# Performance work log

Hardware: AMD Instinct MI355X
Metric: run time of the kernel (lower is better)

Reference implementation:

```python
import jax, jax.numpy as jnp
import numpy as np

D_MODEL = 256
D_STATE = 16
D_CONV = 3
D_INNER = 256          # expand=1
D_HALF = D_INNER // 2  # 128
DT_RANK = 16           # ceil(256/16)
B, L0, L1 = 4, 4096, 4096


def setup_inputs() -> dict:
    key = jax.random.key(0)
    ks = jax.random.split(key, 10)
    u_0 = jax.random.normal(ks[0], (B, L0, D_MODEL), jnp.float32)
    u_1 = jax.random.normal(ks[1], (B, L1, D_MODEL), jnp.float32)
    in_proj_w = jax.random.normal(ks[2], (D_INNER, D_MODEL), jnp.float32) * (D_MODEL ** -0.5)
    conv_x_w = jax.random.normal(ks[3], (D_HALF, 1, D_CONV), jnp.float32) * (D_CONV ** -0.5)
    conv_z_w = jax.random.normal(ks[4], (D_HALF, 1, D_CONV), jnp.float32) * (D_CONV ** -0.5)
    x_proj_w = jax.random.normal(ks[5], (DT_RANK + 2 * D_STATE, D_HALF), jnp.float32) * (D_HALF ** -0.5)
    dt_init_std = DT_RANK ** -0.5
    dt_proj_w = jax.random.uniform(ks[6], (D_HALF, DT_RANK), jnp.float32, -dt_init_std, dt_init_std)
    # dt bias = inverse-softplus of dt ~ LogUniform(1e-3, 1e-1)
    dt = jnp.exp(jax.random.uniform(ks[7], (D_HALF,), jnp.float32) * (np.log(0.1) - np.log(0.001)) + np.log(0.001))
    dt = jnp.clip(dt, 1e-4, None)
    dt_proj_b = dt + jnp.log(-jnp.expm1(-dt))
    A_log = jnp.log(jnp.broadcast_to(jnp.arange(1, D_STATE + 1, dtype=jnp.float32), (D_HALF, D_STATE)))
    D_param = jnp.ones((D_HALF,), jnp.float32)
    out_proj_w = jax.random.normal(ks[8], (D_MODEL, D_INNER), jnp.float32) * (D_INNER ** -0.5)
    return {"u_0": u_0, "u_1": u_1, "in_proj_w": in_proj_w, "conv_x_w": conv_x_w,
            "conv_z_w": conv_z_w, "x_proj_w": x_proj_w, "dt_proj_w": dt_proj_w,
            "dt_proj_b": dt_proj_b, "A_log": A_log, "D": D_param, "out_proj_w": out_proj_w}


def _dwconv(x, w):
    # x: [B, C, L], w: [C, 1, K] depthwise, padding='same', no bias (conv_bias//2 == 0)
    return jax.lax.conv_general_dilated(
        x, w, window_strides=(1,), padding='SAME',
        feature_group_count=x.shape[1], dimension_numbers=('NCH', 'OIH', 'NCH'))


def _selective_scan(u, delta, A, Bm, Cm, Dv):
    # u, delta: [B, L, d]; A: [d, n]; Bm, Cm: [B, L, n]; Dv: [d]
    dA = jnp.exp(delta[..., None] * A)                       # [B, L, d, n]
    dBu = (delta * u)[..., None] * Bm[:, :, None, :]         # [B, L, d, n]
    def combine(c1, c2):
        a1, b1 = c1
        a2, b2 = c2
        return a2 * a1, a2 * b1 + b2
    _, h = jax.lax.associative_scan(combine, (dA, dBu), axis=1)  # h: [B, L, d, n]
    return jnp.einsum('bldn,bln->bld', h, Cm) + u * Dv


def _stream(u, in_proj_w, conv_x_w, conv_z_w, x_proj_w, dt_proj_w, dt_proj_b, A, D, out_proj_w):
    xz = jnp.einsum('bld,ed->ble', u, in_proj_w)             # [B, L, d_inner]
    x, z = jnp.split(xz, 2, axis=-1)                         # [B, L, d_half] each
    x = jnp.swapaxes(x, 1, 2)                                # [B, d_half, L]
    z = jnp.swapaxes(z, 1, 2)
    x_f = jax.nn.silu(_dwconv(x, conv_x_w))
    z_f = jax.nn.silu(_dwconv(z, conv_z_w))
    xf = jnp.swapaxes(x_f, 1, 2)                             # [B, L, d_half]
    dbl = jnp.einsum('bld,ed->ble', xf, x_proj_w)            # [B, L, dt_rank + 2n]
    dt, Bm, Cm = jnp.split(dbl, [DT_RANK, DT_RANK + D_STATE], axis=-1)
    dt = jnp.einsum('blr,dr->bld', dt, dt_proj_w)
    delta = jax.nn.softplus(dt + dt_proj_b)                  # delta_bias + delta_softplus
    y = _selective_scan(xf, delta, A, Bm, Cm, D)             # [B, L, d_half]
    cat = jnp.concatenate([y, jnp.swapaxes(z_f, 1, 2)], axis=-1)  # [B, L, d_inner]
    return jnp.einsum('ble,oe->blo', cat, out_proj_w)


def reference(u_0, u_1, in_proj_w, conv_x_w, conv_z_w, x_proj_w, dt_proj_w, dt_proj_b, A_log, D, out_proj_w):
    A = -jnp.exp(A_log)
    out0 = _stream(u_0, in_proj_w, conv_x_w, conv_z_w, x_proj_w, dt_proj_w, dt_proj_b, A, D, out_proj_w)
    out1 = _stream(u_1, in_proj_w, conv_x_w, conv_z_w, x_proj_w, dt_proj_w, dt_proj_b, A, D, out_proj_w)
    return (out0, out1)
```

## Files before the change

### kernel.cpp

```cpp
#include <hip/hip_runtime.h>
#include <hip/hip_bf16.h>
#include <cstdint>

#define DEV __device__ __forceinline__

typedef __attribute__((ext_vector_type(8))) short short8;
typedef __attribute__((ext_vector_type(4))) float f32x4;
typedef __attribute__((ext_vector_type(4))) unsigned short us4;
typedef __attribute__((ext_vector_type(8))) unsigned short us8;

DEV unsigned short f2bf(float x) {
    unsigned int u = __float_as_uint(x);
    unsigned int r = (u + 0x7FFFu + ((u >> 16) & 1u)) >> 16;
    return (unsigned short)r;
}
DEV float bf2f(unsigned short h) { return __uint_as_float(((unsigned int)h) << 16); }

DEV void gld_lds16(const unsigned short* g, unsigned short* l) {
    __builtin_amdgcn_global_load_lds(
        (const __attribute__((address_space(1))) unsigned int*)g,
        (__attribute__((address_space(3))) unsigned int*)l, 16, 0, 0);
}

#define LL 4096
#define DM 256
#define DH 128
#define NS 16
#define SB_TOT 8
#define CH1 32
#define NCH 128
#define LOG2E 1.44269504088896f

__global__ __launch_bounds__(256) void prep_kernel(
    const float* __restrict__ u0, const float* __restrict__ u1,
    const float* __restrict__ inw, const float* __restrict__ outw,
    const float* __restrict__ xpw, const float* __restrict__ dtw,
    unsigned short* __restrict__ ubf, unsigned short* __restrict__ wbi,
    unsigned short* __restrict__ wbo, unsigned short* __restrict__ Wb)
{
    int gid = blockIdx.x * 256 + threadIdx.x;
    int i = gid * 4;
    if (i < 4194304) {
        f32x4 v = *(const f32x4*)&u0[i];
        us4 r = { f2bf(v.x), f2bf(v.y), f2bf(v.z), f2bf(v.w) };
        *(us4*)&ubf[i] = r;
    } else if (i < 8388608) {
        int j = i - 4194304;
        f32x4 v = *(const f32x4*)&u1[j];
        us4 r = { f2bf(v.x), f2bf(v.y), f2bf(v.z), f2bf(v.w) };
        *(us4*)&ubf[4194304 + j] = r;
    } else if (i < 8454144) {
        int j = i - 8388608;
        f32x4 v = *(const f32x4*)&inw[j];
        us4 r = { f2bf(v.x), f2bf(v.y), f2bf(v.z), f2bf(v.w) };
        *(us4*)&wbi[j] = r;
    } else if (i < 8519680) {
        int j = i - 8454144;
        f32x4 v = *(const f32x4*)&outw[j];
        us4 r = { f2bf(v.x), f2bf(v.y), f2bf(v.z), f2bf(v.w) };
        *(us4*)&wbo[j] = r;
    } else if (i < 8540160) {
        int j = i - 8519680;
        int n = j >> 7, k0 = j & 127;
        if (n < 128) {
            float a0 = 0.f, a1 = 0.f, a2 = 0.f, a3 = 0.f;
            const float* dw = dtw + n * 16;
            #pragma unroll
            for (int r = 0; r < 16; ++r) {
                float w = dw[r];
                const float* xr = xpw + r * 128 + k0;
                a0 = fmaf(w, xr[0], a0);
                a1 = fmaf(w, xr[1], a1);
                a2 = fmaf(w, xr[2], a2);
                a3 = fmaf(w, xr[3], a3);
            }
            us4 rr = { f2bf(a0), f2bf(a1), f2bf(a2), f2bf(a3) };
            *(us4*)&Wb[n * 128 + k0] = rr;
        } else {
            f32x4 v = *(const f32x4*)&xpw[(n - 112) * 128 + k0];
            us4 rr = { f2bf(v.x), f2bf(v.y), f2bf(v.z), f2bf(v.w) };
            *(us4*)&Wb[n * 128 + k0] = rr;
        }
    }
}

template<int F32OUT>
__global__ __launch_bounds__(256) void gemm_bt(
    const unsigned short* __restrict__ A, const unsigned short* __restrict__ B,
    float* __restrict__ Cf, unsigned short* __restrict__ Cb)
{
    __shared__ __align__(16) unsigned short As[128 * 32];
    __shared__ __align__(16) unsigned short Bs[128 * 32];
    const int t = threadIdx.x;
    const int m0 = blockIdx.x * 128, n0 = blockIdx.y * 128;
    const int lane = t & 63, wv = t >> 6;
    const int wm = (wv & 1) * 64, wn = (wv >> 1) * 64;
    const int lr = lane & 15, lk = (lane >> 4) * 8;
    const int srow = lane >> 2, scol = (lane & 3) * 8;

    f32x4 acc[4][4] = {};
    for (int kt = 0; kt < 8; ++kt) {
        const int k0 = kt * 32;
        #pragma unroll
        for (int h = 0; h < 2; ++h) {
            const int c = wv + h * 4;
            const unsigned short* ga = A + (size_t)(m0 + c * 16 + srow) * 256 + k0 + scol;
            const unsigned short* gb = B + (size_t)(n0 + c * 16 + srow) * 256 + k0 + scol;
            gld_lds16(ga, &As[c * 512]);
            gld_lds16(gb, &Bs[c * 512]);
        }
        __syncthreads();
        short8 av[4], bv[4];
        #pragma unroll
        for (int i = 0; i < 4; ++i) av[i] = *(const short8*)&As[(wm + i * 16 + lr) * 32 + lk];
        #pragma unroll
        for (int i = 0; i < 4; ++i) bv[i] = *(const short8*)&Bs[(wn + i * 16 + lr) * 32 + lk];
        #pragma unroll
        for (int i = 0; i < 4; ++i)
            #pragma unroll
            for (int j = 0; j < 4; ++j)
                acc[i][j] = __builtin_amdgcn_mfma_f32_16x16x32_bf16(av[i], bv[j], acc[i][j], 0, 0, 0);
        __syncthreads();
    }
    #pragma unroll
    for (int i = 0; i < 4; ++i) {
        #pragma unroll
        for (int j = 0; j < 4; ++j) {
            int r0 = m0 + wm + i * 16 + (lane >> 4) * 4;
            int cc = n0 + wn + j * 16 + lr;
            #pragma unroll
            for (int r = 0; r < 4; ++r) {
                float v = acc[i][j][r];
                if (F32OUT) Cf[(size_t)(r0 + r) * 256 + cc] = v;
                else        Cb[(size_t)(r0 + r) * 256 + cc] = f2bf(v);
            }
        }
    }
}

__global__ __launch_bounds__(256) void convproj(
    const unsigned short* __restrict__ xz, const unsigned short* __restrict__ Wb,
    const float* __restrict__ wx, const float* __restrict__ wz,
    const float* __restrict__ dtb,
    float* __restrict__ xf, unsigned short* __restrict__ catb,
    float* __restrict__ delta, float* __restrict__ BC)
{
    __shared__ __align__(16) unsigned short Bs[160 * 136];
    __shared__ __align__(16) unsigned short As[64 * 136];
    const int t = threadIdx.x;
    const int m0 = blockIdx.x * 64;
    for (int q = t; q < 2560; q += 256) {
        int n = q >> 4, kc = (q & 15) * 8;
        *(short8*)&Bs[n * 136 + kc] = *(const short8*)(Wb + n * 128 + kc);
    }
    #pragma unroll
    for (int i = 0; i < 8; ++i) {
        int s = t + i * 256;
        int r = s >> 5, g = s & 31;
        int gr = m0 + r;
        int l = gr & 4095;
        int c; const float* wp; const unsigned short* bp;
        if (g < 16) { c = g * 8;        wp = wx; bp = xz + (size_t)gr * 256 + c; }
        else        { c = (g - 16) * 8; wp = wz; bp = xz + (size_t)gr * 256 + 128 + c; }
        us8 zz = (us8)0;
        us8 vm = (l > 0)    ? *(const us8*)(bp - 256) : zz;
        us8 v0 = *(const us8*)bp;
        us8 vp = (l < 4095) ? *(const us8*)(bp + 256) : zz;
        float o[8];
        #pragma unroll
        for (int j = 0; j < 8; ++j) {
            int cc = c + j;
            float v = bf2f(vm[j]) * wp[cc * 3] + bf2f(v0[j]) * wp[cc * 3 + 1]
                    + bf2f(vp[j]) * wp[cc * 3 + 2];
            v = v / (1.f + __expf(-v));
            o[j] = v;
        }
        us8 rb = { f2bf(o[0]), f2bf(o[1]), f2bf(o[2]), f2bf(o[3]),
                   f2bf(o[4]), f2bf(o[5]), f2bf(o[6]), f2bf(o[7]) };
        if (g < 16) {
            *(us8*)&As[r * 136 + c] = rb;
            *(f32x4*)&xf[(size_t)gr * 128 + c]     = *(f32x4*)&o[0];
            *(f32x4*)&xf[(size_t)gr * 128 + c + 4] = *(f32x4*)&o[4];
        } else {
            *(us8*)&catb[(size_t)gr * 256 + 128 + c] = rb;
        }
    }
    __syncthreads();
    const int lane = t & 63, wv = t >> 6;
    const int lr = lane & 15, lk = (lane >> 4) * 8;
    f32x4 acc[10] = {};
    #pragma unroll
    for (int kt = 0; kt < 4; ++kt) {
        const int k0 = kt * 32;
        short8 av = *(const short8*)&As[(wv * 16 + lr) * 136 + k0 + lk];
        #pragma unroll
        for (int j = 0; j < 10; ++j) {
            short8 bv = *(const short8*)&Bs[(j * 16 + lr) * 136 + k0 + lk];
            acc[j] = __builtin_amdgcn_mfma_f32_16x16x32_bf16(av, bv, acc[j], 0, 0, 0);
        }
    }
    const int r0 = (lane >> 4) * 4;
    #pragma unroll
    for (int j = 0; j < 10; ++j) {
        int col = j * 16 + lr;
        #pragma unroll
        for (int r = 0; r < 4; ++r) {
            float v = acc[j][r];
            size_t row = (size_t)m0 + wv * 16 + r0 + r;
            if (j < 8) {
                float x = v + dtb[col];
                float sp = (x > 20.f) ? x : log1pf(__expf(x));
                delta[row * 128 + col] = sp;
            } else {
                BC[row * 32 + (col - 128)] = v;
            }
        }
    }
}

__global__ __launch_bounds__(128) void scan_p1(
    const float* __restrict__ delta, const float* __restrict__ xf,
    const float* __restrict__ BC, const float* __restrict__ alog,
    float* __restrict__ P, float* __restrict__ H)
{
    __shared__ float dt_s[CH1 * 128];
    __shared__ float du_s[CH1 * 128];
    __shared__ float b_s[CH1 * 16];
    int t = threadIdx.x;
    int ch = blockIdx.x, sb = blockIdx.y;
    size_t rb = (size_t)sb * LL + (size_t)ch * CH1;
    for (int q = t; q < CH1 * 32; q += 128) {
        int row = q >> 5, c4 = (q & 31) * 4;
        f32x4 dv = *(const f32x4*)&delta[(rb + row) * DH + c4];
        f32x4 uv = *(const f32x4*)&xf[(rb + row) * DH + c4];
        *(f32x4*)&dt_s[row * 128 + c4] = dv;
        f32x4 duv = dv * uv;
        *(f32x4*)&du_s[row * 128 + c4] = duv;
    }
    {
        int q = t & 127;
        int row = q >> 2, c4 = (q & 3) * 4;
        *(f32x4*)&b_s[row * 16 + c4] = *(const f32x4*)&BC[(rb + row) * 32 + c4];
    }
    __syncthreads();
    float Ar[16];
    #pragma unroll
    for (int n = 0; n < 16; ++n) Ar[n] = -__expf(alog[t * 16 + n]) * LOG2E;
    float h[16], p[16];
    #pragma unroll
    for (int n = 0; n < 16; ++n) { h[n] = 0.f; p[n] = 1.f; }
    for (int i = 0; i < CH1; ++i) {
        float dt = dt_s[i * 128 + t];
        float du = du_s[i * 128 + t];
        float bl[16];
        *(f32x4*)&bl[0]  = *(const f32x4*)&b_s[i * 16];
        *(f32x4*)&bl[4]  = *(const f32x4*)&b_s[i * 16 + 4];
        *(f32x4*)&bl[8]  = *(const f32x4*)&b_s[i * 16 + 8];
        *(f32x4*)&bl[12] = *(const f32x4*)&b_s[i * 16 + 12];
        #pragma unroll
        for (int n = 0; n < 16; ++n) {
            float a = exp2f(dt * Ar[n]);
            h[n] = fmaf(a, h[n], du * bl[n]);
            p[n] *= a;
        }
    }
    size_t ob = (((size_t)sb * NCH + ch) * 128 + t) * 16;
    #pragma unroll
    for (int n4 = 0; n4 < 16; n4 += 4) {
        f32x4 pv = { p[n4], p[n4 + 1], p[n4 + 2], p[n4 + 3] };
        f32x4 hv = { h[n4], h[n4 + 1], h[n4 + 2], h[n4 + 3] };
        *(f32x4*)&P[ob + n4] = pv;
        *(f32x4*)&H[ob + n4] = hv;
    }
}

__global__ __launch_bounds__(256) void scan_p2(const float* __restrict__ P, float* __restrict__ H)
{
    __shared__ float Ps[NCH * 16], Hs[NCH * 16];
    int t = threadIdx.x;
    int d = blockIdx.x, sb = blockIdx.y;
    for (int q = t; q < NCH * 4; q += 256) {
        int ch = q >> 2, c4 = (q & 3) * 4;
        size_t g = (((size_t)sb * NCH + ch) * 128 + d) * 16 + c4;
        *(f32x4*)&Ps[ch * 16 + c4] = *(const f32x4*)&P[g];
        *(f32x4*)&Hs[ch * 16 + c4] = *(const f32x4*)&H[g];
    }
    __syncthreads();
    if (t < 16) {
        float hin = 0.f;
        for (int c = 0; c < NCH; ++c) {
            float pp = Ps[c * 16 + t], hl = Hs[c * 16 + t];
            Hs[c * 16 + t] = hin;
            hin = fmaf(pp, hin, hl);
        }
    }
    __syncthreads();
    for (int q = t; q < NCH * 4; q += 256) {
        int ch = q >> 2, c4 = (q & 3) * 4;
        size_t g = (((size_t)sb * NCH + ch) * 128 + d) * 16 + c4;
        *(f32x4*)&H[g] = *(const f32x4*)&Hs[ch * 16 + c4];
    }
}

__global__ __launch_bounds__(128) void scan_p3(
    const float* __restrict__ delta, const float* __restrict__ xf,
    const float* __restrict__ BC, const float* __restrict__ alog,
    const float* __restrict__ Dp, const float* __restrict__ H,
    unsigned short* __restrict__ catb)
{
    __shared__ float dt_s[CH1 * 128];
    __shared__ float u_s[CH1 * 128];
    __shared__ float b_s[CH1 * 16];
    __shared__ float c_s[CH1 * 16];
    int t = threadIdx.x;
    int ch = blockIdx.x, sb = blockIdx.y;
    size_t rb = (size_t)sb * LL + (size_t)ch * CH1;
    for (int q = t; q < CH1 * 32; q += 128) {
        int row = q >> 5, c4 = (q & 31) * 4;
        *(f32x4*)&dt_s[row * 128 + c4] = *(const f32x4*)&delta[(rb + row) * DH + c4];
        *(f32x4*)&u_s[row * 128 + c4]  = *(const f32x4*)&xf[(rb + row) * DH + c4];
    }
    {
        int q = t & 127;
        int row = q >> 2, c4 = (q & 3) * 4;
        *(f32x4*)&b_s[row * 16 + c4] = *(const f32x4*)&BC[(rb + row) * 32 + c4];
        *(f32x4*)&c_s[row * 16 + c4] = *(const f32x4*)&BC[(rb + row) * 32 + 16 + c4];
    }
    __syncthreads();
    float Ar[16];
    #pragma unroll
    for (int n = 0; n < 16; ++n) Ar[n] = -__expf(alog[t * 16 + n]) * LOG2E;
    float Dv = Dp[t];
    size_t ob = (((size_t)sb * NCH + ch) * 128 + t) * 16;
    float h[16];
    #pragma unroll
    for (int n4 = 0; n4 < 16; n4 += 4) {
        f32x4 hv = *(const f32x4*)&H[ob + n4];
        h[n4] = hv.x; h[n4 + 1] = hv.y; h[n4 + 2] = hv.z; h[n4 + 3] = hv.w;
    }
    for (int i = 0; i < CH1; ++i) {
        float dt = dt_s[i * 128 + t];
        float uu = u_s[i * 128 + t];
        float du = dt * uu;
        float bl[16], cl[16];
        *(f32x4*)&bl[0]  = *(const f32x4*)&b_s[i * 16];
        *(f32x4*)&bl[4]  = *(const f32x4*)&b_s[i * 16 + 4];
        *(f32x4*)&bl[8]  = *(const f32x4*)&b_s[i * 16 + 8];
        *(f32x4*)&bl[12] = *(const f32x4*)&b_s[i * 16 + 12];
        *(f32x4*)&cl[0]  = *(const f32x4*)&c_s[i * 16];
        *(f32x4*)&cl[4]  = *(const f32x4*)&c_s[i * 16 + 4];
        *(f32x4*)&cl[8]  = *(const f32x4*)&c_s[i * 16 + 8];
        *(f32x4*)&cl[12] = *(const f32x4*)&c_s[i * 16 + 12];
        float y0 = uu * Dv, y1 = 0.f, y2 = 0.f, y3 = 0.f;
        #pragma unroll
        for (int n = 0; n < 16; n += 4) {
            float a0 = exp2f(dt * Ar[n]);
            float a1 = exp2f(dt * Ar[n + 1]);
            float a2 = exp2f(dt * Ar[n + 2]);
            float a3 = exp2f(dt * Ar[n + 3]);
            h[n]     = fmaf(a0, h[n],     du * bl[n]);
            h[n + 1] = fmaf(a1, h[n + 1], du * bl[n + 1]);
            h[n + 2] = fmaf(a2, h[n + 2], du * bl[n + 2]);
            h[n + 3] = fmaf(a3, h[n + 3], du * bl[n + 3]);
            y0 = fmaf(h[n],     cl[n],     y0);
            y1 = fmaf(h[n + 1], cl[n + 1], y1);
            y2 = fmaf(h[n + 2], cl[n + 2], y2);
            y3 = fmaf(h[n + 3], cl[n + 3], y3);
        }
        float y = (y0 + y1) + (y2 + y3);
        catb[(rb + i) * DM + t] = f2bf(y);
    }
}

extern "C" void kernel_launch(void* const* d_in, const int* in_sizes, int n_in,
                              void* d_out, int out_size, void* d_ws, size_t ws_size,
                              hipStream_t stream) {
    const float* u0   = (const float*)d_in[0];
    const float* u1   = (const float*)d_in[1];
    const float* inw  = (const float*)d_in[2];
    const float* cxw  = (const float*)d_in[3];
    const float* czw  = (const float*)d_in[4];
    const float* xpw  = (const float*)d_in[5];
    const float* dtw  = (const float*)d_in[6];
    const float* dtb  = (const float*)d_in[7];
    const float* alog = (const float*)d_in[8];
    const float* Dp   = (const float*)d_in[9];
    const float* outw = (const float*)d_in[10];

    char* ws = (char*)d_ws;
    unsigned short* ubf  = (unsigned short*)(ws + 0);
    float* delta         = (float*)(ws + 0);
    unsigned short* xzbf = (unsigned short*)(ws + 16777216);
    float* P             = (float*)(ws + 16777216);
    float* H             = (float*)(ws + 25165824);
    float* xf            = (float*)(ws + 33554432);
    float* BC            = (float*)(ws + 50331648);
    unsigned short* catb = (unsigned short*)(ws + 54525952);
    unsigned short* wbi  = (unsigned short*)(ws + 71303168);
    unsigned short* wbo  = (unsigned short*)(ws + 71434240);
    unsigned short* Wb   = (unsigned short*)(ws + 71565312);

    float* outp = (float*)d_out;

    prep_kernel<<<8340, 256, 0, stream>>>(u0, u1, inw, outw, xpw, dtw, ubf, wbi, wbo, Wb);
    gemm_bt<0><<<dim3(256, 2), 256, 0, stream>>>(ubf, wbi, nullptr, xzbf);
    convproj<<<512, 256, 0, stream>>>(xzbf, Wb, cxw, czw, dtb, xf, catb, delta, BC);
    scan_p1<<<dim3(NCH, 8), 128, 0, stream>>>(delta, xf, BC, alog, P, H);
    scan_p2<<<dim3(128, 8), 256, 0, stream>>>(P, H);
    scan_p3<<<dim3(NCH, 8), 128, 0, stream>>>(delta, xf, BC, alog, Dp, H, catb);
    gemm_bt<1><<<dim3(256, 2), 256, 0, stream>>>(catb, wbo, outp, nullptr);
}
```

Baseline: 224.7 us.

## Fuse all stages into one persistent kernel with grid-wide atomic barriers

Replaces the seven separate launches (prep, two GEMMs, conv/projection, three scan phases) with a single persistent 512-block kernel whose stages are separated by software grid barriers built on atomic counters. It also keeps delta and x in registers between scan phase 1 and phase 3, so they are not reloaded, and reads the projection weights from global memory instead of staging them in LDS. The aim is to remove launch gaps and repeated loads. In exchange the barriers spin and serialize the stages, the barrier is only safe if all 512 blocks are resident at once, and shared-memory reuse through a union may limit occupancy.

```diff
diff --git a/kernel.cpp b/kernel.cpp
--- a/kernel.cpp
+++ b/kernel.cpp
@@ -25,74 +25,44 @@
 #define LL 4096
 #define DM 256
 #define DH 128
-#define NS 16
 #define SB_TOT 8
 #define CH1 32
 #define NCH 128
 #define LOG2E 1.44269504088896f
-
-__global__ __launch_bounds__(256) void prep_kernel(
-    const float* __restrict__ u0, const float* __restrict__ u1,
-    const float* __restrict__ inw, const float* __restrict__ outw,
-    const float* __restrict__ xpw, const float* __restrict__ dtw,
-    unsigned short* __restrict__ ubf, unsigned short* __restrict__ wbi,
-    unsigned short* __restrict__ wbo, unsigned short* __restrict__ Wb)
+#define NBLK 512
+
+DEV void gbar(unsigned int* cnt, int idx) {
+    __syncthreads();
+    if (threadIdx.x == 0) {
+        __threadfence();
+        __hip_atomic_fetch_add(&cnt[idx], 1u, __ATOMIC_ACQ_REL, __HIP_MEMORY_SCOPE_AGENT);
+        while (__hip_atomic_load(&cnt[idx], __ATOMIC_ACQUIRE, __HIP_MEMORY_SCOPE_AGENT) < (unsigned)NBLK) {
+            __builtin_amdgcn_s_sleep(4);
+        }
+        __threadfence();
+    }
+    __syncthreads();
+}
+
+__global__ __launch_bounds__(64) void bar_init(unsigned int* cnt) {
+    if (threadIdx.x < 16) cnt[threadIdx.x] = 0u;
+}
+
+union SMU {
+    struct { unsigned short As[128 * 32]; unsigned short Bs[128 * 32]; } g;
+    struct { unsigned short As[64 * 136]; } c;
+    struct { float b_s[2][512]; float c_s[2][512];
+             float Ps[2][2048]; float Hs[2][2048]; } s;
+};
+
+template<int F32OUT>
+DEV void gemm_phase(SMU* sm, int blk, int t,
+                    const unsigned short* A, const unsigned short* B,
+                    float* Cf, unsigned short* Cb)
 {
-    int gid = blockIdx.x * 256 + threadIdx.x;
-    int i = gid * 4;
-    if (i < 4194304) {
-        f32x4 v = *(const f32x4*)&u0[i];
-        us4 r = { f2bf(v.x), f2bf(v.y), f2bf(v.z), f2bf(v.w) };
-        *(us4*)&ubf[i] = r;
-    } else if (i < 8388608) {
-        int j = i - 4194304;
-        f32x4 v = *(const f32x4*)&u1[j];
-        us4 r = { f2bf(v.x), f2bf(v.y), f2bf(v.z), f2bf(v.w) };
-        *(us4*)&ubf[4194304 + j] = r;
-    } else if (i < 8454144) {
-        int j = i - 8388608;
-        f32x4 v = *(const f32x4*)&inw[j];
-        us4 r = { f2bf(v.x), f2bf(v.y), f2bf(v.z), f2bf(v.w) };
-        *(us4*)&wbi[j] = r;
-    } else if (i < 8519680) {
-        int j = i - 8454144;
-        f32x4 v = *(const f32x4*)&outw[j];
-        us4 r = { f2bf(v.x), f2bf(v.y), f2bf(v.z), f2bf(v.w) };
-        *(us4*)&wbo[j] = r;
-    } else if (i < 8540160) {
-        int j = i - 8519680;
-        int n = j >> 7, k0 = j & 127;
-        if (n < 128) {
-            float a0 = 0.f, a1 = 0.f, a2 = 0.f, a3 = 0.f;
-            const float* dw = dtw + n * 16;
-            #pragma unroll
-            for (int r = 0; r < 16; ++r) {
-                float w = dw[r];
-                const float* xr = xpw + r * 128 + k0;
-                a0 = fmaf(w, xr[0], a0);
-                a1 = fmaf(w, xr[1], a1);
-                a2 = fmaf(w, xr[2], a2);
-                a3 = fmaf(w, xr[3], a3);
-            }
-            us4 rr = { f2bf(a0), f2bf(a1), f2bf(a2), f2bf(a3) };
-            *(us4*)&Wb[n * 128 + k0] = rr;
-        } else {
-            f32x4 v = *(const f32x4*)&xpw[(n - 112) * 128 + k0];
-            us4 rr = { f2bf(v.x), f2bf(v.y), f2bf(v.z), f2bf(v.w) };
-            *(us4*)&Wb[n * 128 + k0] = rr;
-        }
-    }
-}
-
-template<int F32OUT>
-__global__ __launch_bounds__(256) void gemm_bt(
-    const unsigned short* __restrict__ A, const unsigned short* __restrict__ B,
-    float* __restrict__ Cf, unsigned short* __restrict__ Cb)
-{
-    __shared__ __align__(16) unsigned short As[128 * 32];
-    __shared__ __align__(16) unsigned short Bs[128 * 32];
-    const int t = threadIdx.x;
-    const int m0 = blockIdx.x * 128, n0 = blockIdx.y * 128;
+    unsigned short* As = sm->g.As;
+    unsigned short* Bs = sm->g.Bs;
+    const int m0 = (blk >> 1) * 128, n0 = (blk & 1) * 128;
     const int lane = t & 63, wv = t >> 6;
     const int wm = (wv & 1) * 64, wn = (wv >> 1) * 64;
     const int lr = lane & 15, lk = (lane >> 4) * 8;
@@ -138,238 +108,260 @@
     }
 }
 
-__global__ __launch_bounds__(256) void convproj(
-    const unsigned short* __restrict__ xz, const unsigned short* __restrict__ Wb,
-    const float* __restrict__ wx, const float* __restrict__ wz,
-    const float* __restrict__ dtb,
-    float* __restrict__ xf, unsigned short* __restrict__ catb,
-    float* __restrict__ delta, float* __restrict__ BC)
+__global__ __launch_bounds__(256, 2) void mamba_all(
+    const float* u0, const float* u1, const float* inw,
+    const float* cxw, const float* czw, const float* xpw,
+    const float* dtw, const float* dtb, const float* alog,
+    const float* Dp, const float* outw,
+    unsigned short* ubf, unsigned short* wbi, unsigned short* wbo,
+    unsigned short* Wb, unsigned short* xzbf, float* xf,
+    unsigned short* catb, float* delta, float* BC,
+    float* P, float* H, float* outp, unsigned int* cnt)
 {
-    __shared__ __align__(16) unsigned short Bs[160 * 136];
-    __shared__ __align__(16) unsigned short As[64 * 136];
     const int t = threadIdx.x;
-    const int m0 = blockIdx.x * 64;
-    for (int q = t; q < 2560; q += 256) {
-        int n = q >> 4, kc = (q & 15) * 8;
-        *(short8*)&Bs[n * 136 + kc] = *(const short8*)(Wb + n * 128 + kc);
+    const int b = blockIdx.x;
+    __shared__ __align__(16) SMU sm;
+
+    for (int it = 0; it < 17; ++it) {
+        int i = (b * 256 + t + it * 131072) * 4;
+        if (i >= 8540160) break;
+        if (i < 4194304) {
+            f32x4 v = *(const f32x4*)&u0[i];
+            us4 r = { f2bf(v.x), f2bf(v.y), f2bf(v.z), f2bf(v.w) };
+            *(us4*)&ubf[i] = r;
+        } else if (i < 8388608) {
+            int j = i - 4194304;
+            f32x4 v = *(const f32x4*)&u1[j];
+            us4 r = { f2bf(v.x), f2bf(v.y), f2bf(v.z), f2bf(v.w) };
+            *(us4*)&ubf[4194304 + j] = r;
+        } else if (i < 8454144) {
+            int j = i - 8388608;
+            f32x4 v = *(const f32x4*)&inw[j];
+            us4 r = { f2bf(v.x), f2bf(v.y), f2bf(v.z), f2bf(v.w) };
+            *(us4*)&wbi[j] = r;
+        } else if (i < 8519680) {
+            int j = i - 8454144;
+            f32x4 v = *(const f32x4*)&outw[j];
+            us4 r = { f2bf(v.x), f2bf(v.y), f2bf(v.z), f2bf(v.w) };
+            *(us4*)&wbo[j] = r;
+        } else {
+            int j = i - 8519680;
+            int n = j >> 7, k0 = j & 127;
+            if (n < 128) {
+                float a0 = 0.f, a1 = 0.f, a2 = 0.f, a3 = 0.f;
+                const float* dw = dtw + n * 16;
+                #pragma unroll
+                for (int r = 0; r < 16; ++r) {
+                    float w = dw[r];
+                    const float* xr = xpw + r * 128 + k0;
+                    a0 = fmaf(w, xr[0], a0);
+                    a1 = fmaf(w, xr[1], a1);
+                    a2 = fmaf(w, xr[2], a2);
+                    a3 = fmaf(w, xr[3], a3);
+                }
+                us4 rr = { f2bf(a0), f2bf(a1), f2bf(a2), f2bf(a3) };
+                *(us4*)&Wb[n * 128 + k0] = rr;
+            } else {
+                f32x4 v = *(const f32x4*)&xpw[(n - 112) * 128 + k0];
+                us4 rr = { f2bf(v.x), f2bf(v.y), f2bf(v.z), f2bf(v.w) };
+                *(us4*)&Wb[n * 128 + k0] = rr;
+            }
+        }
+    }
+    gbar(cnt, 0);
+
+    gemm_phase<0>(&sm, b, t, ubf, wbi, nullptr, xzbf);
+    gbar(cnt, 1);
+
+    {
+        const int m0 = b * 64;
+        #pragma unroll
+        for (int i = 0; i < 8; ++i) {
+            int s = t + i * 256;
+            int r = s >> 5, g = s & 31;
+            int gr = m0 + r;
+            int l = gr & 4095;
+            int c; const float* wp; const unsigned short* bp;
+            if (g < 16) { c = g * 8;        wp = cxw; bp = xzbf + (size_t)gr * 256 + c; }
+            else        { c = (g - 16) * 8; wp = czw; bp = xzbf + (size_t)gr * 256 + 128 + c; }
+            us8 zz = (us8)0;
+            us8 vm = (l > 0)    ? *(const us8*)(bp - 256) : zz;
+            us8 v0 = *(const us8*)bp;
+            us8 vp = (l < 4095) ? *(const us8*)(bp + 256) : zz;
+            float o[8];
+            #pragma unroll
+            for (int j = 0; j < 8; ++j) {
+                int cc = c + j;
+                float v = bf2f(vm[j]) * wp[cc * 3] + bf2f(v0[j]) * wp[cc * 3 + 1]
+                        + bf2f(vp[j]) * wp[cc * 3 + 2];
+                v = v / (1.f + __expf(-v));
+                o[j] = v;
+            }
+            us8 rb8 = { f2bf(o[0]), f2bf(o[1]), f2bf(o[2]), f2bf(o[3]),
+                        f2bf(o[4]), f2bf(o[5]), f2bf(o[6]), f2bf(o[7]) };
+            if (g < 16) {
+                *(us8*)&sm.c.As[r * 136 + c] = rb8;
+                *(f32x4*)&xf[(size_t)gr * 128 + c]     = *(f32x4*)&o[0];
+                *(f32x4*)&xf[(size_t)gr * 128 + c + 4] = *(f32x4*)&o[4];
+            } else {
+                *(us8*)&catb[(size_t)gr * 256 + 128 + c] = rb8;
+            }
+        }
+        __syncthreads();
+        const int lane = t & 63, wv = t >> 6;
+        const int lr = lane & 15, lk = (lane >> 4) * 8;
+        f32x4 acc[10] = {};
+        #pragma unroll
+        for (int kt = 0; kt < 4; ++kt) {
+            const int k0 = kt * 32;
+            short8 av = *(const short8*)&sm.c.As[(wv * 16 + lr) * 136 + k0 + lk];
+            #pragma unroll
+            for (int j = 0; j < 10; ++j) {
+                short8 bv = *(const short8*)(Wb + (j * 16 + lr) * 128 + k0 + lk);
+                acc[j] = __builtin_amdgcn_mfma_f32_16x16x32_bf16(av, bv, acc[j], 0, 0, 0);
+            }
+        }
+        const int r0 = (lane >> 4) * 4;
+        #pragma unroll
+        for (int j = 0; j < 10; ++j) {
+            int col = j * 16 + lr;
+            #pragma unroll
+            for (int r = 0; r < 4; ++r) {
+                float v = acc[j][r];
+                size_t row = (size_t)m0 + wv * 16 + r0 + r;
+                if (j < 8) {
+                    float x = v + dtb[col];
+                    float sp = (x > 20.f) ? x : log1pf(__expf(x));
+                    delta[row * 128 + col] = sp;
+                } else {
+                    BC[row * 32 + (col - 128)] = v;
+                }
+            }
+        }
+    }
+    gbar(cnt, 2);
+
+    const int hh = t >> 7, tl = t & 127;
+    const int task = 2 * b + hh;
+    const int sb = task >> 7, ch = task & 127;
+    const size_t rb = (size_t)sb * LL + (size_t)ch * CH1;
+    float dtr[32], ur[32];
+    {
+        int row = tl >> 2, c4 = (tl & 3) * 4;
+        *(f32x4*)&sm.s.b_s[hh][row * 16 + c4] = *(const f32x4*)&BC[(rb + row) * 32 + c4];
+        *(f32x4*)&sm.s.c_s[hh][row * 16 + c4] = *(const f32x4*)&BC[(rb + row) * 32 + 16 + c4];
     }
     #pragma unroll
-    for (int i = 0; i < 8; ++i) {
-        int s = t + i * 256;
-        int r = s >> 5, g = s & 31;
-        int gr = m0 + r;
-        int l = gr & 4095;
-        int c; const float* wp; const unsigned short* bp;
-        if (g < 16) { c = g * 8;        wp = wx; bp = xz + (size_t)gr * 256 + c; }
-        else        { c = (g - 16) * 8; wp = wz; bp = xz + (size_t)gr * 256 + 128 + c; }
-        us8 zz = (us8)0;
-        us8 vm = (l > 0)    ? *(const us8*)(bp - 256) : zz;
-        us8 v0 = *(const us8*)bp;
-        us8 vp = (l < 4095) ? *(const us8*)(bp + 256) : zz;
-        float o[8];
-        #pragma unroll
-        for (int j = 0; j < 8; ++j) {
-            int cc = c + j;
-            float v = bf2f(vm[j]) * wp[cc * 3] + bf2f(v0[j]) * wp[cc * 3 + 1]
-                    + bf2f(vp[j]) * wp[cc * 3 + 2];
-            v = v / (1.f + __expf(-v));
-            o[j] = v;
-        }
-        us8 rb = { f2bf(o[0]), f2bf(o[1]), f2bf(o[2]), f2bf(o[3]),
-                   f2bf(o[4]), f2bf(o[5]), f2bf(o[6]), f2bf(o[7]) };
-        if (g < 16) {
-            *(us8*)&As[r * 136 + c] = rb;
-            *(f32x4*)&xf[(size_t)gr * 128 + c]     = *(f32x4*)&o[0];
-            *(f32x4*)&xf[(size_t)gr * 128 + c + 4] = *(f32x4*)&o[4];
-        } else {
-            *(us8*)&catb[(size_t)gr * 256 + 128 + c] = rb;
-        }
-    }
+    for (int i = 0; i < 32; ++i) dtr[i] = delta[(rb + i) * DH + tl];
+    #pragma unroll
+    for (int i = 0; i < 32; ++i) ur[i] = xf[(rb + i) * DH + tl];
     __syncthreads();
-    const int lane = t & 63, wv = t >> 6;
-    const int lr = lane & 15, lk = (lane >> 4) * 8;
-    f32x4 acc[10] = {};
-    #pragma unroll
-    for (int kt = 0; kt < 4; ++kt) {
-        const int k0 = kt * 32;
-        short8 av = *(const short8*)&As[(wv * 16 + lr) * 136 + k0 + lk];
-        #pragma unroll
-        for (int j = 0; j < 10; ++j) {
-            short8 bv = *(const short8*)&Bs[(j * 16 + lr) * 136 + k0 + lk];
-            acc[j] = __builtin_amdgcn_mfma_f32_16x16x32_bf16(av, bv, acc[j], 0, 0, 0);
-        }
-    }
-    const int r0 = (lane >> 4) * 4;
-    #pragma unroll
-    for (int j = 0; j < 10; ++j) {
-        int col = j * 16 + lr;
-        #pragma unroll
-        for (int r = 0; r < 4; ++r) {
-            float v = acc[j][r];
-            size_t row = (size_t)m0 + wv * 16 + r0 + r;
-            if (j < 8) {
-                float x = v + dtb[col];
-                float sp = (x > 20.f) ? x : log1pf(__expf(x));
-                delta[row * 128 + col] = sp;
-            } else {
-                BC[row * 32 + (col - 128)] = v;
-            }
-        }
-    }
-}
-
-__global__ __launch_bounds__(128) void scan_p1(
-    const float* __restrict__ delta, const float* __restrict__ xf,
-    const float* __restrict__ BC, const float* __restrict__ alog,
-    float* __restrict__ P, float* __restrict__ H)
-{
-    __shared__ float dt_s[CH1 * 128];
-    __shared__ float du_s[CH1 * 128];
-    __shared__ float b_s[CH1 * 16];
-    int t = threadIdx.x;
-    int ch = blockIdx.x, sb = blockIdx.y;
-    size_t rb = (size_t)sb * LL + (size_t)ch * CH1;
-    for (int q = t; q < CH1 * 32; q += 128) {
-        int row = q >> 5, c4 = (q & 31) * 4;
-        f32x4 dv = *(const f32x4*)&delta[(rb + row) * DH + c4];
-        f32x4 uv = *(const f32x4*)&xf[(rb + row) * DH + c4];
-        *(f32x4*)&dt_s[row * 128 + c4] = dv;
-        f32x4 duv = dv * uv;
-        *(f32x4*)&du_s[row * 128 + c4] = duv;
-    }
     {
-        int q = t & 127;
-        int row = q >> 2, c4 = (q & 3) * 4;
-        *(f32x4*)&b_s[row * 16 + c4] = *(const f32x4*)&BC[(rb + row) * 32 + c4];
-    }
-    __syncthreads();
-    float Ar[16];
-    #pragma unroll
-    for (int n = 0; n < 16; ++n) Ar[n] = -__expf(alog[t * 16 + n]) * LOG2E;
-    float h[16], p[16];
-    #pragma unroll
-    for (int n = 0; n < 16; ++n) { h[n] = 0.f; p[n] = 1.f; }
-    for (int i = 0; i < CH1; ++i) {
-        float dt = dt_s[i * 128 + t];
-        float du = du_s[i * 128 + t];
-        float bl[16];
-        *(f32x4*)&bl[0]  = *(const f32x4*)&b_s[i * 16];
-        *(f32x4*)&bl[4]  = *(const f32x4*)&b_s[i * 16 + 4];
-        *(f32x4*)&bl[8]  = *(const f32x4*)&b_s[i * 16 + 8];
-        *(f32x4*)&bl[12] = *(const f32x4*)&b_s[i * 16 + 12];
-        #pragma unroll
-        for (int n = 0; n < 16; ++n) {
-            float a = exp2f(dt * Ar[n]);
-            h[n] = fmaf(a, h[n], du * bl[n]);
-            p[n] *= a;
-        }
-    }
-    size_t ob = (((size_t)sb * NCH + ch) * 128 + t) * 16;
-    #pragma unroll
-    for (int n4 = 0; n4 < 16; n4 += 4) {
-        f32x4 pv = { p[n4], p[n4 + 1], p[n4 + 2], p[n4 + 3] };
-        f32x4 hv = { h[n4], h[n4 + 1], h[n4 + 2], h[n4 + 3] };
-        *(f32x4*)&P[ob + n4] = pv;
-        *(f32x4*)&H[ob + n4] = hv;
-    }
-}
-
-__global__ __launch_bounds__(256) void scan_p2(const float* __restrict__ P, float* __restrict__ H)
-{
-    __shared__ float Ps[NCH * 16], Hs[NCH * 16];
-    int t = threadIdx.x;
-    int d = blockIdx.x, sb = blockIdx.y;
-    for (int q = t; q < NCH * 4; q += 256) {
-        int ch = q >> 2, c4 = (q & 3) * 4;
-        size_t g = (((size_t)sb * NCH + ch) * 128 + d) * 16 + c4;
-        *(f32x4*)&Ps[ch * 16 + c4] = *(const f32x4*)&P[g];
-        *(f32x4*)&Hs[ch * 16 + c4] = *(const f32x4*)&H[g];
-    }
-    __syncthreads();
-    if (t < 16) {
-        float hin = 0.f;
-        for (int c = 0; c < NCH; ++c) {
-            float pp = Ps[c * 16 + t], hl = Hs[c * 16 + t];
-            Hs[c * 16 + t] = hin;
-            hin = fmaf(pp, hin, hl);
-        }
-    }
-    __syncthreads();
-    for (int q = t; q < NCH * 4; q += 256) {
-        int ch = q >> 2, c4 = (q & 3) * 4;
-        size_t g = (((size_t)sb * NCH + ch) * 128 + d) * 16 + c4;
-        *(f32x4*)&H[g] = *(const f32x4*)&Hs[ch * 16 + c4];
-    }
-}
-
-__global__ __launch_bounds__(128) void scan_p3(
-    const float* __restrict__ delta, const float* __restrict__ xf,
-    const float* __restrict__ BC, const float* __restrict__ alog,
-    const float* __restrict__ Dp, const float* __restrict__ H,
-    unsigned short* __restrict__ catb)
-{
-    __shared__ float dt_s[CH1 * 128];
-    __shared__ float u_s[CH1 * 128];
-    __shared__ float b_s[CH1 * 16];
-    __shared__ float c_s[CH1 * 16];
-    int t = threadIdx.x;
-    int ch = blockIdx.x, sb = blockIdx.y;
-    size_t rb = (size_t)sb * LL + (size_t)ch * CH1;
-    for (int q = t; q < CH1 * 32; q += 128) {
-        int row = q >> 5, c4 = (q & 31) * 4;
-        *(f32x4*)&dt_s[row * 128 + c4] = *(const f32x4*)&delta[(rb + row) * DH + c4];
-        *(f32x4*)&u_s[row * 128 + c4]  = *(const f32x4*)&xf[(rb + row) * DH + c4];
-    }
+        float Ar[16];
+        #pragma unroll
+        for (int n = 0; n < 16; ++n) Ar[n] = -__expf(alog[tl * 16 + n]) * LOG2E;
+        float h[16], p[16];
+        #pragma unroll
+        for (int n = 0; n < 16; ++n) { h[n] = 0.f; p[n] = 1.f; }
+        for (int i = 0; i < CH1; ++i) {
+            float dt = dtr[i];
+            float du = dt * ur[i];
+            float bl[16];
+            *(f32x4*)&bl[0]  = *(const f32x4*)&sm.s.b_s[hh][i * 16];
+            *(f32x4*)&bl[4]  = *(const f32x4*)&sm.s.b_s[hh][i * 16 + 4];
+            *(f32x4*)&bl[8]  = *(const f32x4*)&sm.s.b_s[hh][i * 16 + 8];
+            *(f32x4*)&bl[12] = *(const f32x4*)&sm.s.b_s[hh][i * 16 + 12];
+            #pragma unroll
+            for (int n = 0; n < 16; ++n) {
+                float a = exp2f(dt * Ar[n]);
+                h[n] = fmaf(a, h[n], du * bl[n]);
+                p[n] *= a;
+            }
+        }
+        size_t ob = (((size_t)sb * NCH + ch) * 128 + tl) * 16;
+        #pragma unroll
+        for (int n4 = 0; n4 < 16; n4 += 4) {
+            f32x4 pv = { p[n4], p[n4 + 1], p[n4 + 2], p[n4 + 3] };
+            f32x4 hv = { h[n4], h[n4 + 1], h[n4 + 2], h[n4 + 3] };
+            *(f32x4*)&P[ob + n4] = pv;
+            *(f32x4*)&H[ob + n4] = hv;
+        }
+    }
+    gbar(cnt, 3);
+
     {
-        int q = t & 127;
-        int row = q >> 2, c4 = (q & 3) * 4;
-        *(f32x4*)&b_s[row * 16 + c4] = *(const f32x4*)&BC[(rb + row) * 32 + c4];
-        *(f32x4*)&c_s[row * 16 + c4] = *(const f32x4*)&BC[(rb + row) * 32 + 16 + c4];
-    }
-    __syncthreads();
-    float Ar[16];
-    #pragma unroll
-    for (int n = 0; n < 16; ++n) Ar[n] = -__expf(alog[t * 16 + n]) * LOG2E;
-    float Dv = Dp[t];
-    size_t ob = (((size_t)sb * NCH + ch) * 128 + t) * 16;
-    float h[16];
-    #pragma unroll
-    for (int n4 = 0; n4 < 16; n4 += 4) {
-        f32x4 hv = *(const f32x4*)&H[ob + n4];
-        h[n4] = hv.x; h[n4 + 1] = hv.y; h[n4 + 2] = hv.z; h[n4 + 3] = hv.w;
-    }
-    for (int i = 0; i < CH1; ++i) {
-        float dt = dt_s[i * 128 + t];
-        float uu = u_s[i * 128 + t];
-        float du = dt * uu;
-        float bl[16], cl[16];
-        *(f32x4*)&bl[0]  = *(const f32x4*)&b_s[i * 16];
-        *(f32x4*)&bl[4]  = *(const f32x4*)&b_s[i * 16 + 4];
-        *(f32x4*)&bl[8]  = *(const f32x4*)&b_s[i * 16 + 8];
-        *(f32x4*)&bl[12] = *(const f32x4*)&b_s[i * 16 + 12];
-        *(f32x4*)&cl[0]  = *(const f32x4*)&c_s[i * 16];
-        *(f32x4*)&cl[4]  = *(const f32x4*)&c_s[i * 16 + 4];
-        *(f32x4*)&cl[8]  = *(const f32x4*)&c_s[i * 16 + 8];
-        *(f32x4*)&cl[12] = *(const f32x4*)&c_s[i * 16 + 12];
-        float y0 = uu * Dv, y1 = 0.f, y2 = 0.f, y3 = 0.f;
-        #pragma unroll
-        for (int n = 0; n < 16; n += 4) {
-            float a0 = exp2f(dt * Ar[n]);
-            float a1 = exp2f(dt * Ar[n + 1]);
-            float a2 = exp2f(dt * Ar[n + 2]);
-            float a3 = exp2f(dt * Ar[n + 3]);
-            h[n]     = fmaf(a0, h[n],     du * bl[n]);
-            h[n + 1] = fmaf(a1, h[n + 1], du * bl[n + 1]);
-            h[n + 2] = fmaf(a2, h[n + 2], du * bl[n + 2]);
-            h[n + 3] = fmaf(a3, h[n + 3], du * bl[n + 3]);
-            y0 = fmaf(h[n],     cl[n],     y0);
-            y1 = fmaf(h[n + 1], cl[n + 1], y1);
-            y2 = fmaf(h[n + 2], cl[n + 2], y2);
-            y3 = fmaf(h[n + 3], cl[n + 3], y3);
-        }
-        float y = (y0 + y1) + (y2 + y3);
-        catb[(rb + i) * DM + t] = f2bf(y);
-    }
+        const int sb2 = task >> 7, d2 = task & 127;
+        size_t g0 = (((size_t)sb2 * NCH + tl) * 128 + d2) * 16;
+        #pragma unroll
+        for (int n4 = 0; n4 < 16; n4 += 4) {
+            *(f32x4*)&sm.s.Ps[hh][tl * 16 + n4] = *(const f32x4*)&P[g0 + n4];
+            *(f32x4*)&sm.s.Hs[hh][tl * 16 + n4] = *(const f32x4*)&H[g0 + n4];
+        }
+        __syncthreads();
+        if (tl < 16) {
+            float hin = 0.f;
+            for (int c2 = 0; c2 < NCH; ++c2) {
+                float pp = sm.s.Ps[hh][c2 * 16 + tl];
+                float hl = sm.s.Hs[hh][c2 * 16 + tl];
+                sm.s.Hs[hh][c2 * 16 + tl] = hin;
+                hin = fmaf(pp, hin, hl);
+            }
+        }
+        __syncthreads();
+        #pragma unroll
+        for (int n4 = 0; n4 < 16; n4 += 4)
+            *(f32x4*)&H[g0 + n4] = *(const f32x4*)&sm.s.Hs[hh][tl * 16 + n4];
+    }
+    gbar(cnt, 4);
+
+    {
+        float Ar[16];
+        #pragma unroll
+        for (int n = 0; n < 16; ++n) Ar[n] = -__expf(alog[tl * 16 + n]) * LOG2E;
+        float Dv = Dp[tl];
+        size_t ob = (((size_t)sb * NCH + ch) * 128 + tl) * 16;
+        float h[16];
+        #pragma unroll
+        for (int n4 = 0; n4 < 16; n4 += 4) {
+            f32x4 hv = *(const f32x4*)&H[ob + n4];
+            h[n4] = hv.x; h[n4 + 1] = hv.y; h[n4 + 2] = hv.z; h[n4 + 3] = hv.w;
+        }
+        for (int i = 0; i < CH1; ++i) {
+            float dt = dtr[i];
+            float uu = ur[i];
+            float du = dt * uu;
+            float bl[16], cl[16];
+            *(f32x4*)&bl[0]  = *(const f32x4*)&sm.s.b_s[hh][i * 16];
+            *(f32x4*)&bl[4]  = *(const f32x4*)&sm.s.b_s[hh][i * 16 + 4];
+            *(f32x4*)&bl[8]  = *(const f32x4*)&sm.s.b_s[hh][i * 16 + 8];
+            *(f32x4*)&bl[12] = *(const f32x4*)&sm.s.b_s[hh][i * 16 + 12];
+            *(f32x4*)&cl[0]  = *(const f32x4*)&sm.s.c_s[hh][i * 16];
+            *(f32x4*)&cl[4]  = *(const f32x4*)&sm.s.c_s[hh][i * 16 + 4];
+            *(f32x4*)&cl[8]  = *(const f32x4*)&sm.s.c_s[hh][i * 16 + 8];
+            *(f32x4*)&cl[12] = *(const f32x4*)&sm.s.c_s[hh][i * 16 + 12];
+            float y0 = uu * Dv, y1 = 0.f, y2 = 0.f, y3 = 0.f;
+            #pragma unroll
+            for (int n = 0; n < 16; n += 4) {
+                float a0 = exp2f(dt * Ar[n]);
+                float a1 = exp2f(dt * Ar[n + 1]);
+                float a2 = exp2f(dt * Ar[n + 2]);
+                float a3 = exp2f(dt * Ar[n + 3]);
+                h[n]     = fmaf(a0, h[n],     du * bl[n]);
+                h[n + 1] = fmaf(a1, h[n + 1], du * bl[n + 1]);
+                h[n + 2] = fmaf(a2, h[n + 2], du * bl[n + 2]);
+                h[n + 3] = fmaf(a3, h[n + 3], du * bl[n + 3]);
+                y0 = fmaf(h[n],     cl[n],     y0);
+                y1 = fmaf(h[n + 1], cl[n + 1], y1);
+                y2 = fmaf(h[n + 2], cl[n + 2], y2);
+                y3 = fmaf(h[n + 3], cl[n + 3], y3);
+            }
+            float y = (y0 + y1) + (y2 + y3);
+            catb[(rb + i) * DM + tl] = f2bf(y);
+        }
+    }
+    gbar(cnt, 5);
+
+    gemm_phase<1>(&sm, b, t, catb, wbo, outp, nullptr);
 }
 
 extern "C" void kernel_launch(void* const* d_in, const int* in_sizes, int n_in,
@@ -399,14 +391,13 @@
     unsigned short* wbi  = (unsigned short*)(ws + 71303168);
     unsigned short* wbo  = (unsigned short*)(ws + 71434240);
     unsigned short* Wb   = (unsigned short*)(ws + 71565312);
+    unsigned int*   cnt  = (unsigned int*)(ws + 71606272);
 
     float* outp = (float*)d_out;
 
-    prep_kernel<<<8340, 256, 0, stream>>>(u0, u1, inw, outw, xpw, dtw, ubf, wbi, wbo, Wb);
-    gemm_bt<0><<<dim3(256, 2), 256, 0, stream>>>(ubf, wbi, nullptr, xzbf);
-    convproj<<<512, 256, 0, stream>>>(xzbf, Wb, cxw, czw, dtb, xf, catb, delta, BC);
-    scan_p1<<<dim3(NCH, 8), 128, 0, stream>>>(delta, xf, BC, alog, P, H);
-    scan_p2<<<dim3(128, 8), 256, 0, stream>>>(P, H);
-    scan_p3<<<dim3(NCH, 8), 128, 0, stream>>>(delta, xf, BC, alog, Dp, H, catb);
-    gemm_bt<1><<<dim3(256, 2), 256, 0, stream>>>(catb, wbo, outp, nullptr);
-}
+    bar_init<<<1, 64, 0, stream>>>(cnt);
+    mamba_all<<<NBLK, 256, 0, stream>>>(
+        u0, u1, inw, cxw, czw, xpw, dtw, dtb, alog, Dp, outw,
+        ubf, wbi, wbo, Wb, xzbf, xf, catb, delta, BC,
+        (float*)P, (float*)H, outp, cnt);
+}
```

New measurement: 645.7 us. +187.4%, slower.

## Fuse chunk-local scan pass into conv/projection kernel

Applied to the files above, without the earlier changes.

Adds a templated variant of the conv+x_proj kernel that, after computing delta and B, runs the first selective-scan pass (per-chunk decay products and local states) directly in the same block. The B values are kept in shared memory, and the scan_p1 launch is dropped when the workspace is large enough for separate P/H buffers placed past the existing layout. This removes a kernel launch and avoids re-reading B from global memory. Delta and xf are still reread from global, though likely L2-resident. Only 512 blocks run the serial scan, and the per-thread register pressure of the fused kernel grows.

```diff
diff --git a/kernel.cpp b/kernel.cpp
--- a/kernel.cpp
+++ b/kernel.cpp
@@ -25,7 +25,6 @@
 #define LL 4096
 #define DM 256
 #define DH 128
-#define NS 16
 #define SB_TOT 8
 #define CH1 32
 #define NCH 128
@@ -138,15 +137,18 @@
     }
 }
 
-__global__ __launch_bounds__(256) void convproj(
+template<int FUSE_SCAN>
+__global__ __launch_bounds__(256) void convproj_k(
     const unsigned short* __restrict__ xz, const unsigned short* __restrict__ Wb,
     const float* __restrict__ wx, const float* __restrict__ wz,
-    const float* __restrict__ dtb,
+    const float* __restrict__ dtb, const float* __restrict__ alog,
     float* __restrict__ xf, unsigned short* __restrict__ catb,
-    float* __restrict__ delta, float* __restrict__ BC)
+    float* __restrict__ delta, float* __restrict__ BC,
+    float* __restrict__ P, float* __restrict__ H)
 {
     __shared__ __align__(16) unsigned short Bs[160 * 136];
     __shared__ __align__(16) unsigned short As[64 * 136];
+    __shared__ float bc_s[64 * 16];
     const int t = threadIdx.x;
     const int m0 = blockIdx.x * 64;
     for (int q = t; q < 2560; q += 256) {
@@ -175,14 +177,14 @@
             v = v / (1.f + __expf(-v));
             o[j] = v;
         }
-        us8 rb = { f2bf(o[0]), f2bf(o[1]), f2bf(o[2]), f2bf(o[3]),
-                   f2bf(o[4]), f2bf(o[5]), f2bf(o[6]), f2bf(o[7]) };
+        us8 rb8 = { f2bf(o[0]), f2bf(o[1]), f2bf(o[2]), f2bf(o[3]),
+                    f2bf(o[4]), f2bf(o[5]), f2bf(o[6]), f2bf(o[7]) };
         if (g < 16) {
-            *(us8*)&As[r * 136 + c] = rb;
+            *(us8*)&As[r * 136 + c] = rb8;
             *(f32x4*)&xf[(size_t)gr * 128 + c]     = *(f32x4*)&o[0];
             *(f32x4*)&xf[(size_t)gr * 128 + c + 4] = *(f32x4*)&o[4];
         } else {
-            *(us8*)&catb[(size_t)gr * 256 + 128 + c] = rb;
+            *(us8*)&catb[(size_t)gr * 256 + 128 + c] = rb8;
         }
     }
     __syncthreads();
@@ -206,15 +208,54 @@
         #pragma unroll
         for (int r = 0; r < 4; ++r) {
             float v = acc[j][r];
-            size_t row = (size_t)m0 + wv * 16 + r0 + r;
+            int lrow = wv * 16 + r0 + r;
+            size_t row = (size_t)m0 + lrow;
             if (j < 8) {
                 float x = v + dtb[col];
                 float sp = (x > 20.f) ? x : log1pf(__expf(x));
                 delta[row * 128 + col] = sp;
             } else {
                 BC[row * 32 + (col - 128)] = v;
+                if (FUSE_SCAN && j == 8) bc_s[lrow * 16 + lr] = v;
             }
         }
+    }
+    if (!FUSE_SCAN) return;
+
+    __syncthreads();
+    const int hh = t >> 7, tl = t & 127;
+    const int sb = m0 >> 12;
+    const int ch = ((m0 & 4095) >> 5) + hh;
+    const size_t rb = (size_t)m0 + hh * 32;
+    float Ar[16];
+    #pragma unroll
+    for (int n = 0; n < 16; ++n) Ar[n] = -__expf(alog[tl * 16 + n]) * LOG2E;
+    float h[16], p[16];
+    #pragma unroll
+    for (int n = 0; n < 16; ++n) { h[n] = 0.f; p[n] = 1.f; }
+    for (int i = 0; i < CH1; ++i) {
+        float dt = delta[(rb + i) * DH + tl];
+        float uu = xf[(rb + i) * DH + tl];
+        float du = dt * uu;
+        float bl[16];
+        *(f32x4*)&bl[0]  = *(const f32x4*)&bc_s[(hh * 32 + i) * 16];
+        *(f32x4*)&bl[4]  = *(const f32x4*)&bc_s[(hh * 32 + i) * 16 + 4];
+        *(f32x4*)&bl[8]  = *(const f32x4*)&bc_s[(hh * 32 + i) * 16 + 8];
+        *(f32x4*)&bl[12] = *(const f32x4*)&bc_s[(hh * 32 + i) * 16 + 12];
+        #pragma unroll
+        for (int n = 0; n < 16; ++n) {
+            float a = exp2f(dt * Ar[n]);
+            h[n] = fmaf(a, h[n], du * bl[n]);
+            p[n] *= a;
+        }
+    }
+    size_t ob = (((size_t)sb * NCH + ch) * 128 + tl) * 16;
+    #pragma unroll
+    for (int n4 = 0; n4 < 16; n4 += 4) {
+        f32x4 pv = { p[n4], p[n4 + 1], p[n4 + 2], p[n4 + 3] };
+        f32x4 hv = { h[n4], h[n4 + 1], h[n4 + 2], h[n4 + 3] };
+        *(f32x4*)&P[ob + n4] = pv;
+        *(f32x4*)&H[ob + n4] = hv;
     }
 }
 
@@ -391,22 +432,33 @@
     unsigned short* ubf  = (unsigned short*)(ws + 0);
     float* delta         = (float*)(ws + 0);
     unsigned short* xzbf = (unsigned short*)(ws + 16777216);
-    float* P             = (float*)(ws + 16777216);
-    float* H             = (float*)(ws + 25165824);
+    float* P_a           = (float*)(ws + 16777216);
+    float* H_a           = (float*)(ws + 25165824);
     float* xf            = (float*)(ws + 33554432);
     float* BC            = (float*)(ws + 50331648);
     unsigned short* catb = (unsigned short*)(ws + 54525952);
     unsigned short* wbi  = (unsigned short*)(ws + 71303168);
     unsigned short* wbo  = (unsigned short*)(ws + 71434240);
     unsigned short* Wb   = (unsigned short*)(ws + 71565312);
+    float* P_f           = (float*)(ws + 71606272);
+    float* H_f           = (float*)(ws + 79994880);
 
     float* outp = (float*)d_out;
 
     prep_kernel<<<8340, 256, 0, stream>>>(u0, u1, inw, outw, xpw, dtw, ubf, wbi, wbo, Wb);
     gemm_bt<0><<<dim3(256, 2), 256, 0, stream>>>(ubf, wbi, nullptr, xzbf);
-    convproj<<<512, 256, 0, stream>>>(xzbf, Wb, cxw, czw, dtb, xf, catb, delta, BC);
-    scan_p1<<<dim3(NCH, 8), 128, 0, stream>>>(delta, xf, BC, alog, P, H);
-    scan_p2<<<dim3(128, 8), 256, 0, stream>>>(P, H);
-    scan_p3<<<dim3(NCH, 8), 128, 0, stream>>>(delta, xf, BC, alog, Dp, H, catb);
+
+    if (ws_size >= 88383488ull) {
+        convproj_k<1><<<512, 256, 0, stream>>>(xzbf, Wb, cxw, czw, dtb, alog,
+                                               xf, catb, delta, BC, P_f, H_f);
+        scan_p2<<<dim3(128, 8), 256, 0, stream>>>(P_f, H_f);
+        scan_p3<<<dim3(NCH, 8), 128, 0, stream>>>(delta, xf, BC, alog, Dp, H_f, catb);
+    } else {
+        convproj_k<0><<<512, 256, 0, stream>>>(xzbf, Wb, cxw, czw, dtb, alog,
+                                               xf, catb, delta, BC, nullptr, nullptr);
+        scan_p1<<<dim3(NCH, 8), 128, 0, stream>>>(delta, xf, BC, alog, P_a, H_a);
+        scan_p2<<<dim3(128, 8), 256, 0, stream>>>(P_a, H_a);
+        scan_p3<<<dim3(NCH, 8), 128, 0, stream>>>(delta, xf, BC, alog, Dp, H_a, catb);
+    }
     gemm_bt<1><<<dim3(256, 2), 256, 0, stream>>>(catb, wbo, outp, nullptr);
 }
```

Result: faster. 219.9 us (-2.1%).
